# Kernel tuning notes

Hardware: AMD Instinct MI355X
Metric: run time of the kernel (lower is better)

## Reference

```python
import jax, jax.numpy as jnp
import numpy as np

NUM_HEADS = 4
NUM_GROUPS = 8
EPS = 1e-5


def group_norm(x, w, b):
    # x: [N, C, H, W], normalize over (C//G, H, W) per group
    N, C, H, W = x.shape
    xg = x.reshape(N, NUM_GROUPS, C // NUM_GROUPS, H, W)
    mu = jnp.mean(xg, axis=(2, 3, 4), keepdims=True)
    var = jnp.var(xg, axis=(2, 3, 4), keepdims=True)
    xn = ((xg - mu) * jax.lax.rsqrt(var + EPS)).reshape(N, C, H, W)
    return xn * w[None, :, None, None] + b[None, :, None, None]


def conv1x1(x, w, b):
    # x: [N, C, H, W], w: [Cout, Cin], b: [Cout]
    return jnp.einsum('nchw,dc->ndhw', x, w) + b[None, :, None, None]


def setup_inputs() -> dict:
    key = jax.random.key(0)
    ks = jax.random.split(key, 12)
    N, C, H, W = 2, 256, 64, 64
    s = 1.0 / np.sqrt(C)
    inp = {
        'x': jax.random.normal(ks[0], (N, C, H, W), jnp.float32),
        'mask': jax.random.randint(ks[1], (N, 1, H, W), 0, 2, jnp.int32),
        'norm_w': jnp.ones((C,), jnp.float32),
        'norm_b': jnp.zeros((C,), jnp.float32),
        'q_w': jax.random.normal(ks[2], (C, C), jnp.float32) * s,
        'q_b': jnp.zeros((C,), jnp.float32),
        'k_w': jax.random.normal(ks[3], (C, C), jnp.float32) * s,
        'k_b': jnp.zeros((C,), jnp.float32),
        'v_w': jax.random.normal(ks[4], (C, C), jnp.float32) * s,
        'v_b': jnp.zeros((C,), jnp.float32),
        'p_w': jax.random.normal(ks[5], (C, C), jnp.float32) * s,
        'p_b': jnp.zeros((C,), jnp.float32),
    }
    return inp


def reference(x, mask, norm_w, norm_b, q_w, q_b, k_w, k_b, v_w, v_b, p_w, p_b):
    N, C, H, W = x.shape
    hd = C // NUM_HEADS  # head dim
    L = H * W
    xn = group_norm(x, norm_w, norm_b)
    q = conv1x1(xn, q_w, q_b).reshape(N, NUM_HEADS, hd, L)
    k = conv1x1(xn, k_w, k_b).reshape(N, NUM_HEADS, hd, L)
    v = conv1x1(xn, v_w, v_b).reshape(N, NUM_HEADS, hd, L)
    scores = jnp.einsum('nhcl,nhck->nhlk', q, k) * (hd ** -0.5)
    probs = jax.nn.softmax(scores, axis=-1)
    out = jnp.einsum('nhlk,nhck->nhcl', probs, v).reshape(N, C, H, W)
    out = conv1x1(out, p_w, p_b)
    return (x + out, mask)
```

## Files before the change

### kernel.cpp

```cpp
#include <hip/hip_runtime.h>
#include <hip/hip_bf16.h>

#define NBATCH 2
#define CCH    256
#define LLEN   4096
#define NGROUP 8
#define CPG    32
#define NHEAD  4
#define HD     64
#define GEPS   1e-5f
#define QSCALE 0.18033688011112042f


typedef short bf16x8 __attribute__((ext_vector_type(8)));
typedef float f32x4  __attribute__((ext_vector_type(4)));

__device__ __forceinline__ unsigned short f2b(float f) {
  unsigned u = __float_as_uint(f);
  u += 0x7FFFu + ((u >> 16) & 1u);
  return (unsigned short)(u >> 16);
}
__device__ __forceinline__ unsigned pack2bf(float a, float b) {
  __hip_bfloat162 h = __float22bfloat162_rn(make_float2(a, b));
  union { __hip_bfloat162 h; unsigned u; } c;
  c.h = h;
  return c.u;
}
__device__ __forceinline__ float exp2_(float x) {
#if __has_builtin(__builtin_amdgcn_exp2f)
  return __builtin_amdgcn_exp2f(x);
#else
  return exp2f(x);
#endif
}

__global__ __launch_bounds__(256) void setup_kernel(
    const float* __restrict__ qw, const float* __restrict__ kw,
    const float* __restrict__ vw, const float* __restrict__ pw,
    const float* __restrict__ qb, const float* __restrict__ kb,
    const float* __restrict__ vb, const float* __restrict__ pb,
    const float* __restrict__ x, const int* __restrict__ mask,
    unsigned short* __restrict__ w16, float* __restrict__ bias_ws,
    float* __restrict__ part, float* __restrict__ out2) {
  __shared__ float rs[4], rss[4];
  const int b = blockIdx.x;
  const int t = threadIdx.x;
  if (b < 256) {
    const int idx = b * 256 + t;
    const int m = idx >> 14;
    const int rem = idx & 16383;
    const int cout = rem >> 6;
    const int ch4 = (rem & 63) << 2;
    const float* src[4] = {qw, kw, vw, pw};
    const float sc = (m == 0) ? QSCALE : 1.0f;
    const float4 v = ((const float4*)src[m])[(size_t)cout * 64 + (ch4 >> 2)];
    unsigned short* dst = w16 +
        ((size_t)(m * 16 + (cout >> 4)) * 8 + (ch4 >> 5)) * 512 +
        ((cout & 15) + 16 * ((ch4 >> 3) & 3)) * 8 + (ch4 & 7);
    dst[0] = f2b(v.x * sc); dst[1] = f2b(v.y * sc);
    dst[2] = f2b(v.z * sc); dst[3] = f2b(v.w * sc);
    if (b == 0) {
      bias_ws[t]       = qb[t] * QSCALE;
      bias_ws[256 + t] = kb[t];
      bias_ws[512 + t] = vb[t];
      bias_ws[768 + t] = pb[t];
    }
  } else if (b < 384) {
    const int sb = b - 256;
    const int gidx = sb >> 3, sub = sb & 7;
    const float4* xp = (const float4*)(x + (size_t)gidx * (CPG * LLEN)) + (size_t)sub * 4096;
    float s = 0.f, ss = 0.f;
    for (int i = t; i < 4096; i += 256) {
      const float4 v = xp[i];
      s += v.x + v.y + v.z + v.w;
      ss = fmaf(v.x, v.x, ss);
      ss = fmaf(v.y, v.y, ss);
      ss = fmaf(v.z, v.z, ss);
      ss = fmaf(v.w, v.w, ss);
    }
#pragma unroll
    for (int off = 32; off; off >>= 1) {
      s  += __shfl_down(s, off);
      ss += __shfl_down(ss, off);
    }
    if ((t & 63) == 0) { rs[t >> 6] = s; rss[t >> 6] = ss; }
    __syncthreads();
    if (t == 0) {
      part[sb * 2 + 0] = rs[0] + rs[1] + rs[2] + rs[3];
      part[sb * 2 + 1] = rss[0] + rss[1] + rss[2] + rss[3];
    }
  } else {
    const int i = (b - 384) * 256 + t;
    out2[i] = (float)mask[i];
  }
}

__global__ __launch_bounds__(256) void gn_apply_kernel(const float* __restrict__ x,
                                                       const float* __restrict__ w,
                                                       const float* __restrict__ b,
                                                       const float* __restrict__ part,
                                                       unsigned short* __restrict__ xn16) {
  const int l0 = blockIdx.x * 32, c0 = blockIdx.y * 32, n = blockIdx.z;
  const int g16 = n * 8 + (c0 >> 5);
  float s = 0.f, ss = 0.f;
#pragma unroll
  for (int i = 0; i < 8; i++) {
    s  += part[(g16 * 8 + i) * 2 + 0];
    ss += part[(g16 * 8 + i) * 2 + 1];
  }
  const float inv_cnt = 1.0f / (float)(CPG * LLEN);
  const float mu = s * inv_cnt;
  const float rsg = rsqrtf(ss * inv_cnt - mu * mu + GEPS);
  __shared__ float tile[32][33];
  const int tx = threadIdx.x & 31, ty = threadIdx.x >> 5;
#pragma unroll
  for (int i = 0; i < 4; i++) {
    const int c = c0 + ty + 8 * i;
    const float wc = w[c], bc = b[c];
    const float v = x[((size_t)n * CCH + c) * LLEN + l0 + tx];
    tile[ty + 8 * i][tx] = (v - mu) * rsg * wc + bc;
  }
  __syncthreads();
  const int c = c0 + tx;
#pragma unroll
  for (int i = 0; i < 4; i++) {
    const int l = l0 + ty + 8 * i;
    const size_t pos = (((size_t)n * 256 + (l >> 4)) * 8 + (c >> 5)) * 512 +
                       ((l & 15) + 16 * ((c >> 3) & 3)) * 8 + (c & 7);
    xn16[pos] = f2b(tile[tx][ty + 8 * i]);
  }
}

__global__ __launch_bounds__(256, 4) void qkv_mfma_kernel(
    const unsigned short* __restrict__ xn16,
    const unsigned short* __restrict__ w16,
    const float* __restrict__ bias_ws,
    unsigned short* __restrict__ q16,
    unsigned short* __restrict__ k16,
    unsigned short* __restrict__ v16) {
  const int t = threadIdx.x;
  const int lane = t & 63, wv = t >> 6;
  const int col = lane & 15, quad = lane >> 4;
  const int m0 = blockIdx.x * 64;
  const int by = blockIdx.y;
  const int co0 = by * 64;
  const int wsel = blockIdx.z;
  const int n = m0 >> 12;
  const int m16b = (m0 & 4095) >> 4;

  const unsigned short* xnb = xn16 + (size_t)n * (256 * 8 * 512);
  const unsigned short* wb  = w16 + ((size_t)(wsel * 16 + by * 4 + wv) * 8) * 512 + lane * 8;

  f32x4 acc[4];
#pragma unroll
  for (int i = 0; i < 4; i++) acc[i] = {0.f, 0.f, 0.f, 0.f};

#pragma unroll
  for (int kc = 0; kc < 8; kc++) {
    const bf16x8 wf = *(const bf16x8*)(wb + (size_t)kc * 512);
#pragma unroll
    for (int mt = 0; mt < 4; mt++) {
      const bf16x8 xf = *(const bf16x8*)(xnb + ((size_t)(m16b + mt) * 8 + kc) * 512 + lane * 8);
      acc[mt] = (wsel < 2)
          ? __builtin_amdgcn_mfma_f32_16x16x32_bf16(xf, wf, acc[mt], 0, 0, 0)
          : __builtin_amdgcn_mfma_f32_16x16x32_bf16(wf, xf, acc[mt], 0, 0, 0);
    }
  }

  if (wsel < 2) {
    unsigned short* dst = (wsel == 0) ? q16 : k16;
    const float bias = bias_ws[wsel * CCH + co0 + wv * 16 + col];
    const int lquad = (wv * 2 + (col >> 3)) & 3;
    const int j = col & 7;
#pragma unroll
    for (int mt = 0; mt < 4; mt++) {
      const size_t base = ((size_t)(n * 256 + m16b + mt) * 8 + by * 2 + (wv >> 1)) * 512 + j;
#pragma unroll
      for (int r = 0; r < 4; r++)
        dst[base + ((quad * 4 + r) + 16 * lquad) * 8] = f2b(acc[mt][r] + bias);
    }
  } else {
    const int l0 = m0 & 4095;
    const int j = col & 7;
#pragma unroll
    for (int ct = 0; ct < 4; ct++) {
      const size_t base = ((size_t)(n * 128 + (l0 >> 5) + (ct >> 1)) * 16 + by * 4 + wv) * 512 +
                          16 * (((ct & 1) << 1) + (col >> 3)) * 8 + j;
#pragma unroll
      for (int r = 0; r < 4; r++) {
        const int cout = co0 + wv * 16 + quad * 4 + r;
        v16[base + (quad * 4 + r) * 8] = f2b(acc[ct][r] + bias_ws[2 * CCH + cout]);
      }
    }
  }
}

__global__ __launch_bounds__(256, 2) void attn_mfma_kernel(
    const unsigned short* __restrict__ q16,
    const unsigned short* __restrict__ k16,
    const unsigned short* __restrict__ v16,
    unsigned short* __restrict__ o16) {
  __shared__ __align__(16) unsigned char shraw[20480];
  unsigned short (*pT)[64][40] = (unsigned short (*)[64][40])shraw;
  f32x4 (*red)[4][64] = (f32x4 (*)[4][64])shraw;
  f32x4 (*lred)[64] = (f32x4 (*)[64])(shraw + 16384);
  const int t = threadIdx.x;
  const int lane = t & 63, wv = t >> 6;
  const int col = lane & 15, quad = lane >> 4;
  const int q0 = blockIdx.x * 64;
  const int n = blockIdx.y >> 2, h = blockIdx.y & 3;
  const int hc = h * HD;

  const unsigned short* qb = q16 + (size_t)n * (256 * 8 * 512);
  const unsigned short* kb = k16 + (size_t)n * (256 * 8 * 512);
  const unsigned short* vb = v16 + (size_t)n * (128 * 16 * 512);

  bf16x8 bq[4][2];
#pragma unroll
  for (int qt = 0; qt < 4; qt++)
#pragma unroll
    for (int ks = 0; ks < 2; ks++)
      bq[qt][ks] = *(const bf16x8*)(qb + ((size_t)(blockIdx.x * 4 + qt) * 8 + h * 2 + ks) * 512 + lane * 8);

  bf16x8 bones;
#pragma unroll
  for (int i = 0; i < 8; i++) bones[i] = (short)0x3F80;

  f32x4 o[4][4], lacc[4];
#pragma unroll
  for (int qt = 0; qt < 4; qt++) {
    lacc[qt] = {0.f, 0.f, 0.f, 0.f};
#pragma unroll
    for (int ct = 0; ct < 4; ct++) o[qt][ct] = {0.f, 0.f, 0.f, 0.f};
  }

  auto ldK = [&](int kc0, int kt, int ks) {
    return *(const bf16x8*)(kb + ((size_t)((kc0 >> 4) + kt) * 8 + h * 2 + ks) * 512 + lane * 8);
  };
  auto ldV = [&](int kc0, int ct) {
    return *(const bf16x8*)(vb + ((size_t)(kc0 >> 5) * 16 + h * 4 + ct) * 512 + lane * 8);
  };

  int kc0 = wv * 1024;
  bf16x8 ka[2][2], bv[4];
#pragma unroll
  for (int kt = 0; kt < 2; kt++)
#pragma unroll
    for (int ks = 0; ks < 2; ks++) ka[kt][ks] = ldK(kc0, kt, ks);
#pragma unroll
  for (int ct = 0; ct < 4; ct++) bv[ct] = ldV(kc0, ct);

  for (int chunk = 0; chunk < 32; chunk++) {
    const int kn = (chunk < 31) ? kc0 + 32 : kc0;
    bf16x8 nka[2][2], nbv[4];
#pragma unroll
    for (int kt = 0; kt < 2; kt++)
#pragma unroll
      for (int ks = 0; ks < 2; ks++) nka[kt][ks] = ldK(kn, kt, ks);
#pragma unroll
    for (int ct = 0; ct < 4; ct++) nbv[ct] = ldV(kn, ct);

#pragma unroll
    for (int kt = 0; kt < 2; kt++)
#pragma unroll
      for (int qt = 0; qt < 4; qt++) {
        f32x4 s = {0.f, 0.f, 0.f, 0.f};
        s = __builtin_amdgcn_mfma_f32_16x16x32_bf16(ka[kt][0], bq[qt][0], s, 0, 0, 0);
        s = __builtin_amdgcn_mfma_f32_16x16x32_bf16(ka[kt][1], bq[qt][1], s, 0, 0, 0);
        uint2 w;
        w.x = pack2bf(exp2_(s[0]), exp2_(s[1]));
        w.y = pack2bf(exp2_(s[2]), exp2_(s[3]));
        *(uint2*)&pT[wv][qt * 16 + col][kt * 16 + quad * 4] = w;
      }
#pragma unroll
    for (int qt = 0; qt < 4; qt++) {
      const bf16x8 pa = *(const bf16x8*)&pT[wv][qt * 16 + col][quad * 8];
      lacc[qt] = __builtin_amdgcn_mfma_f32_16x16x32_bf16(pa, bones, lacc[qt], 0, 0, 0);
#pragma unroll
      for (int ct = 0; ct < 4; ct++)
        o[qt][ct] = __builtin_amdgcn_mfma_f32_16x16x32_bf16(pa, bv[ct], o[qt][ct], 0, 0, 0);
    }
#pragma unroll
    for (int kt = 0; kt < 2; kt++)
#pragma unroll
      for (int ks = 0; ks < 2; ks++) ka[kt][ks] = nka[kt][ks];
#pragma unroll
    for (int ct = 0; ct < 4; ct++) bv[ct] = nbv[ct];
    kc0 = kn;
  }

  const int cch = hc + wv * 16 + col;
  const int lquad16 = 16 * ((cch >> 3) & 3);
  const size_t ctile = cch >> 5;
#pragma unroll
  for (int qt = 0; qt < 4; qt++) {
    __syncthreads();
#pragma unroll
    for (int ct = 0; ct < 4; ct++) red[wv][ct][lane] = o[qt][ct];
    lred[wv][lane] = lacc[qt];
    __syncthreads();
    f32x4 os = red[0][wv][lane];
    os += red[1][wv][lane];
    os += red[2][wv][lane];
    os += red[3][wv][lane];
    f32x4 ls = lred[0][lane];
    ls += lred[1][lane];
    ls += lred[2][lane];
    ls += lred[3][lane];
    const size_t base = (((size_t)n * 256 + blockIdx.x * 4 + qt) * 8 + ctile) * 512 + (cch & 7);
#pragma unroll
    for (int r = 0; r < 4; r++)
      o16[base + ((quad * 4 + r) + lquad16) * 8] = f2b(os[r] / ls[r]);
  }
}

__global__ __launch_bounds__(256, 4) void proj_mfma_kernel(
    const unsigned short* __restrict__ o16,
    const unsigned short* __restrict__ w16,
    const float* __restrict__ pbias,
    const float* __restrict__ x,
    float* __restrict__ out) {
  const int t = threadIdx.x;
  const int lane = t & 63, wv = t >> 6;
  const int col = lane & 15, quad = lane >> 4;
  const int m0 = blockIdx.x * 64;
  const int by = blockIdx.y;
  const int co0 = by * 64;
  const int n = m0 >> 12, l0 = m0 & 4095;

  const unsigned short* ob = o16 + (size_t)n * (256 * 8 * 512);
  const unsigned short* wb = w16 + ((size_t)(48 + by * 4 + wv) * 8) * 512 + lane * 8;

  f32x4 acc[4];
#pragma unroll
  for (int i = 0; i < 4; i++) acc[i] = {0.f, 0.f, 0.f, 0.f};

#pragma unroll
  for (int kc = 0; kc < 8; kc++) {
    const bf16x8 aw = *(const bf16x8*)(wb + (size_t)kc * 512);
#pragma unroll
    for (int lt = 0; lt < 4; lt++) {
      const bf16x8 bo = *(const bf16x8*)(ob + ((size_t)((l0 >> 4) + lt) * 8 + kc) * 512 + lane * 8);
      acc[lt] = __builtin_amdgcn_mfma_f32_16x16x32_bf16(aw, bo, acc[lt], 0, 0, 0);
    }
  }
#pragma unroll
  for (int lt = 0; lt < 4; lt++)
#pragma unroll
    for (int r = 0; r < 4; r++) {
      const int cout = co0 + wv * 16 + quad * 4 + r;
      const size_t idx = ((size_t)(n * CCH + cout)) * LLEN + l0 + lt * 16 + col;
      out[idx] = acc[lt][r] + pbias[cout] + x[idx];
    }
}

extern "C" void kernel_launch(void* const* d_in, const int* in_sizes, int n_in,
                              void* d_out, int out_size, void* d_ws, size_t ws_size,
                              hipStream_t stream) {
  (void)in_sizes; (void)n_in; (void)out_size; (void)ws_size;
  const float* x      = (const float*)d_in[0];
  const int*   mask   = (const int*)d_in[1];
  const float* norm_w = (const float*)d_in[2];
  const float* norm_b = (const float*)d_in[3];
  const float* q_w    = (const float*)d_in[4];
  const float* q_b    = (const float*)d_in[5];
  const float* k_w    = (const float*)d_in[6];
  const float* k_b    = (const float*)d_in[7];
  const float* v_w    = (const float*)d_in[8];
  const float* v_b    = (const float*)d_in[9];
  const float* p_w    = (const float*)d_in[10];
  const float* p_b    = (const float*)d_in[11];

  const size_t TSZ = (size_t)NBATCH * LLEN * CCH;
  unsigned short* xn16 = (unsigned short*)d_ws;
  unsigned short* q16  = xn16 + TSZ;
  unsigned short* k16  = q16 + TSZ;
  unsigned short* v16  = k16 + TSZ;
  unsigned short* o16  = v16 + TSZ;
  unsigned short* w16  = o16 + TSZ;
  float* bias_ws = (float*)(w16 + 4 * 65536);
  float* part    = bias_ws + 1024;

  float* out  = (float*)d_out;
  float* out2 = out + TSZ;

  setup_kernel<<<416, 256, 0, stream>>>(q_w, k_w, v_w, p_w, q_b, k_b, v_b, p_b,
                                        x, mask, w16, bias_ws, part, out2);
  gn_apply_kernel<<<dim3(LLEN / 32, CCH / 32, NBATCH), 256, 0, stream>>>(
      x, norm_w, norm_b, part, xn16);
  qkv_mfma_kernel<<<dim3((NBATCH * LLEN) / 64, CCH / 64, 3), 256, 0, stream>>>(
      xn16, w16, bias_ws, q16, k16, v16);
  attn_mfma_kernel<<<dim3(LLEN / 64, NBATCH * NHEAD), 256, 0, stream>>>(
      q16, k16, v16, o16);
  proj_mfma_kernel<<<dim3((NBATCH * LLEN) / 64, CCH / 64), 256, 0, stream>>>(
      o16, w16, bias_ws + 768, x, out);
}
```

Before: 154.4 us.

## Halve attention and projection tiles, vectorize groupnorm apply, double-buffer K loads

Attention blocks now cover 32 queries instead of 64, doubling the grid to 1024 blocks. Occupancy is raised to 4 blocks per CU, block IDs are remapped so consecutive blocks share the same head, and the K/V prefetch becomes an explicit ping-pong double buffer. Projection tiles are halved to 32 rows, groupnorm stats are split across more blocks, and gn_apply uses float4 loads with packed bf16x8 stores. The goal is better CU fill on a 256-CU part and cheaper memory traffic, at the cost of less K/V reuse per block and more redundant K/V reads.

```diff
diff --git a/kernel.cpp b/kernel.cpp
--- a/kernel.cpp
+++ b/kernel.cpp
@@ -65,12 +65,12 @@
       bias_ws[512 + t] = vb[t];
       bias_ws[768 + t] = pb[t];
     }
-  } else if (b < 384) {
+  } else if (b < 512) {
     const int sb = b - 256;
-    const int gidx = sb >> 3, sub = sb & 7;
-    const float4* xp = (const float4*)(x + (size_t)gidx * (CPG * LLEN)) + (size_t)sub * 4096;
+    const int gidx = sb >> 4, sub = sb & 15;
+    const float4* xp = (const float4*)(x + (size_t)gidx * (CPG * LLEN)) + (size_t)sub * 2048;
     float s = 0.f, ss = 0.f;
-    for (int i = t; i < 4096; i += 256) {
+    for (int i = t; i < 2048; i += 256) {
       const float4 v = xp[i];
       s += v.x + v.y + v.z + v.w;
       ss = fmaf(v.x, v.x, ss);
@@ -90,7 +90,7 @@
       part[sb * 2 + 1] = rss[0] + rss[1] + rss[2] + rss[3];
     }
   } else {
-    const int i = (b - 384) * 256 + t;
+    const int i = (b - 512) * 256 + t;
     out2[i] = (float)mask[i];
   }
 }
@@ -100,35 +100,42 @@
                                                        const float* __restrict__ b,
                                                        const float* __restrict__ part,
                                                        unsigned short* __restrict__ xn16) {
-  const int l0 = blockIdx.x * 32, c0 = blockIdx.y * 32, n = blockIdx.z;
-  const int g16 = n * 8 + (c0 >> 5);
+  const int l0 = blockIdx.x * 64, c0 = blockIdx.y * 32, n = blockIdx.z;
+  const int g16 = n * 8 + blockIdx.y;
   float s = 0.f, ss = 0.f;
 #pragma unroll
-  for (int i = 0; i < 8; i++) {
-    s  += part[(g16 * 8 + i) * 2 + 0];
-    ss += part[(g16 * 8 + i) * 2 + 1];
+  for (int i = 0; i < 16; i++) {
+    s  += part[(g16 * 16 + i) * 2 + 0];
+    ss += part[(g16 * 16 + i) * 2 + 1];
   }
   const float inv_cnt = 1.0f / (float)(CPG * LLEN);
   const float mu = s * inv_cnt;
   const float rsg = rsqrtf(ss * inv_cnt - mu * mu + GEPS);
-  __shared__ float tile[32][33];
-  const int tx = threadIdx.x & 31, ty = threadIdx.x >> 5;
-#pragma unroll
-  for (int i = 0; i < 4; i++) {
-    const int c = c0 + ty + 8 * i;
-    const float wc = w[c], bc = b[c];
-    const float v = x[((size_t)n * CCH + c) * LLEN + l0 + tx];
-    tile[ty + 8 * i][tx] = (v - mu) * rsg * wc + bc;
+  __shared__ float tile[32][68];
+  const int t = threadIdx.x;
+  const int cl = t >> 3, l8 = t & 7;
+  const float aa = rsg * w[c0 + cl];
+  const float dd = b[c0 + cl] - mu * aa;
+  const float* xrow = x + ((size_t)n * CCH + c0 + cl) * LLEN + l0;
+#pragma unroll
+  for (int i = 0; i < 2; i++) {
+    const int ll = (l8 + 8 * i) * 4;
+    float4 v = *(const float4*)(xrow + ll);
+    v.x = fmaf(v.x, aa, dd);
+    v.y = fmaf(v.y, aa, dd);
+    v.z = fmaf(v.z, aa, dd);
+    v.w = fmaf(v.w, aa, dd);
+    *(float4*)&tile[cl][ll] = v;
   }
   __syncthreads();
-  const int c = c0 + tx;
-#pragma unroll
-  for (int i = 0; i < 4; i++) {
-    const int l = l0 + ty + 8 * i;
-    const size_t pos = (((size_t)n * 256 + (l >> 4)) * 8 + (c >> 5)) * 512 +
-                       ((l & 15) + 16 * ((c >> 3) & 3)) * 8 + (c & 7);
-    xn16[pos] = f2b(tile[tx][ty + 8 * i]);
-  }
+  const int l = t & 63, cg = t >> 6;
+  const int labs = l0 + l;
+  bf16x8 ov;
+#pragma unroll
+  for (int j = 0; j < 8; j++) ov[j] = (short)f2b(tile[cg * 8 + j][l]);
+  const size_t pos = (((size_t)n * 256 + (labs >> 4)) * 8 + (c0 >> 5)) * 512 +
+                     ((labs & 15) + 16 * cg) * 8;
+  *(bf16x8*)(xn16 + pos) = ov;
 }
 
 __global__ __launch_bounds__(256, 4) void qkv_mfma_kernel(
@@ -195,40 +202,42 @@
   }
 }
 
-__global__ __launch_bounds__(256, 2) void attn_mfma_kernel(
+__global__ __launch_bounds__(256, 4) void attn_mfma_kernel(
     const unsigned short* __restrict__ q16,
     const unsigned short* __restrict__ k16,
     const unsigned short* __restrict__ v16,
     unsigned short* __restrict__ o16) {
   __shared__ __align__(16) unsigned char shraw[20480];
-  unsigned short (*pT)[64][40] = (unsigned short (*)[64][40])shraw;
+  unsigned short (*pT)[32][40] = (unsigned short (*)[32][40])shraw;
   f32x4 (*red)[4][64] = (f32x4 (*)[4][64])shraw;
   f32x4 (*lred)[64] = (f32x4 (*)[64])(shraw + 16384);
   const int t = threadIdx.x;
   const int lane = t & 63, wv = t >> 6;
   const int col = lane & 15, quad = lane >> 4;
-  const int q0 = blockIdx.x * 64;
-  const int n = blockIdx.y >> 2, h = blockIdx.y & 3;
+  const int fid = blockIdx.y * gridDim.x + blockIdx.x;
+  const int nh = fid & 7, qx = fid >> 3;
+  const int n = nh >> 2, h = nh & 3;
   const int hc = h * HD;
+  const int qt0 = qx * 2;
 
   const unsigned short* qb = q16 + (size_t)n * (256 * 8 * 512);
   const unsigned short* kb = k16 + (size_t)n * (256 * 8 * 512);
   const unsigned short* vb = v16 + (size_t)n * (128 * 16 * 512);
 
-  bf16x8 bq[4][2];
-#pragma unroll
-  for (int qt = 0; qt < 4; qt++)
+  bf16x8 bq[2][2];
+#pragma unroll
+  for (int qt = 0; qt < 2; qt++)
 #pragma unroll
     for (int ks = 0; ks < 2; ks++)
-      bq[qt][ks] = *(const bf16x8*)(qb + ((size_t)(blockIdx.x * 4 + qt) * 8 + h * 2 + ks) * 512 + lane * 8);
+      bq[qt][ks] = *(const bf16x8*)(qb + ((size_t)(qt0 + qt) * 8 + h * 2 + ks) * 512 + lane * 8);
 
   bf16x8 bones;
 #pragma unroll
   for (int i = 0; i < 8; i++) bones[i] = (short)0x3F80;
 
-  f32x4 o[4][4], lacc[4];
-#pragma unroll
-  for (int qt = 0; qt < 4; qt++) {
+  f32x4 o[2][4], lacc[2];
+#pragma unroll
+  for (int qt = 0; qt < 2; qt++) {
     lacc[qt] = {0.f, 0.f, 0.f, 0.f};
 #pragma unroll
     for (int ct = 0; ct < 4; ct++) o[qt][ct] = {0.f, 0.f, 0.f, 0.f};
@@ -241,59 +250,56 @@
     return *(const bf16x8*)(vb + ((size_t)(kc0 >> 5) * 16 + h * 4 + ct) * 512 + lane * 8);
   };
 
-  int kc0 = wv * 1024;
-  bf16x8 ka[2][2], bv[4];
-#pragma unroll
-  for (int kt = 0; kt < 2; kt++)
-#pragma unroll
-    for (int ks = 0; ks < 2; ks++) ka[kt][ks] = ldK(kc0, kt, ks);
-#pragma unroll
-  for (int ct = 0; ct < 4; ct++) bv[ct] = ldV(kc0, ct);
-
-  for (int chunk = 0; chunk < 32; chunk++) {
-    const int kn = (chunk < 31) ? kc0 + 32 : kc0;
-    bf16x8 nka[2][2], nbv[4];
+  bf16x8 kA[2][2], kB[2][2], bv[4];
+  auto loadK = [&](bf16x8 (&kr)[2][2], int kc0) {
 #pragma unroll
     for (int kt = 0; kt < 2; kt++)
 #pragma unroll
-      for (int ks = 0; ks < 2; ks++) nka[kt][ks] = ldK(kn, kt, ks);
-#pragma unroll
-    for (int ct = 0; ct < 4; ct++) nbv[ct] = ldV(kn, ct);
-
+      for (int ks = 0; ks < 2; ks++) kr[kt][ks] = ldK(kc0, kt, ks);
+  };
+  auto loadV = [&](int kc0) {
+#pragma unroll
+    for (int ct = 0; ct < 4; ct++) bv[ct] = ldV(kc0, ct);
+  };
+  auto chunk = [&](bf16x8 (&kr)[2][2]) {
 #pragma unroll
     for (int kt = 0; kt < 2; kt++)
 #pragma unroll
-      for (int qt = 0; qt < 4; qt++) {
+      for (int qt = 0; qt < 2; qt++) {
         f32x4 s = {0.f, 0.f, 0.f, 0.f};
-        s = __builtin_amdgcn_mfma_f32_16x16x32_bf16(ka[kt][0], bq[qt][0], s, 0, 0, 0);
-        s = __builtin_amdgcn_mfma_f32_16x16x32_bf16(ka[kt][1], bq[qt][1], s, 0, 0, 0);
-        uint2 w;
-        w.x = pack2bf(exp2_(s[0]), exp2_(s[1]));
-        w.y = pack2bf(exp2_(s[2]), exp2_(s[3]));
-        *(uint2*)&pT[wv][qt * 16 + col][kt * 16 + quad * 4] = w;
+        s = __builtin_amdgcn_mfma_f32_16x16x32_bf16(kr[kt][0], bq[qt][0], s, 0, 0, 0);
+        s = __builtin_amdgcn_mfma_f32_16x16x32_bf16(kr[kt][1], bq[qt][1], s, 0, 0, 0);
+        uint2 pw;
+        pw.x = pack2bf(exp2_(s[0]), exp2_(s[1]));
+        pw.y = pack2bf(exp2_(s[2]), exp2_(s[3]));
+        *(uint2*)&pT[wv][qt * 16 + col][kt * 16 + quad * 4] = pw;
       }
 #pragma unroll
-    for (int qt = 0; qt < 4; qt++) {
+    for (int qt = 0; qt < 2; qt++) {
       const bf16x8 pa = *(const bf16x8*)&pT[wv][qt * 16 + col][quad * 8];
       lacc[qt] = __builtin_amdgcn_mfma_f32_16x16x32_bf16(pa, bones, lacc[qt], 0, 0, 0);
 #pragma unroll
       for (int ct = 0; ct < 4; ct++)
         o[qt][ct] = __builtin_amdgcn_mfma_f32_16x16x32_bf16(pa, bv[ct], o[qt][ct], 0, 0, 0);
     }
-#pragma unroll
-    for (int kt = 0; kt < 2; kt++)
-#pragma unroll
-      for (int ks = 0; ks < 2; ks++) ka[kt][ks] = nka[kt][ks];
-#pragma unroll
-    for (int ct = 0; ct < 4; ct++) bv[ct] = nbv[ct];
-    kc0 = kn;
+  };
+
+  const int kb0 = wv * 1024;
+  loadK(kA, kb0);
+  for (int it = 0; it < 32; it += 2) {
+    loadV(kb0 + it * 32);
+    loadK(kB, kb0 + (it + 1) * 32);
+    chunk(kA);
+    loadV(kb0 + (it + 1) * 32);
+    loadK(kA, kb0 + ((it + 2 < 32) ? (it + 2) * 32 : (it + 1) * 32));
+    chunk(kB);
   }
 
   const int cch = hc + wv * 16 + col;
   const int lquad16 = 16 * ((cch >> 3) & 3);
   const size_t ctile = cch >> 5;
 #pragma unroll
-  for (int qt = 0; qt < 4; qt++) {
+  for (int qt = 0; qt < 2; qt++) {
     __syncthreads();
 #pragma unroll
     for (int ct = 0; ct < 4; ct++) red[wv][ct][lane] = o[qt][ct];
@@ -307,7 +313,7 @@
     ls += lred[1][lane];
     ls += lred[2][lane];
     ls += lred[3][lane];
-    const size_t base = (((size_t)n * 256 + blockIdx.x * 4 + qt) * 8 + ctile) * 512 + (cch & 7);
+    const size_t base = (((size_t)n * 256 + qt0 + qt) * 8 + ctile) * 512 + (cch & 7);
 #pragma unroll
     for (int r = 0; r < 4; r++)
       o16[base + ((quad * 4 + r) + lquad16) * 8] = f2b(os[r] / ls[r]);
@@ -323,7 +329,7 @@
   const int t = threadIdx.x;
   const int lane = t & 63, wv = t >> 6;
   const int col = lane & 15, quad = lane >> 4;
-  const int m0 = blockIdx.x * 64;
+  const int m0 = blockIdx.x * 32;
   const int by = blockIdx.y;
   const int co0 = by * 64;
   const int n = m0 >> 12, l0 = m0 & 4095;
@@ -331,21 +337,21 @@
   const unsigned short* ob = o16 + (size_t)n * (256 * 8 * 512);
   const unsigned short* wb = w16 + ((size_t)(48 + by * 4 + wv) * 8) * 512 + lane * 8;
 
-  f32x4 acc[4];
-#pragma unroll
-  for (int i = 0; i < 4; i++) acc[i] = {0.f, 0.f, 0.f, 0.f};
+  f32x4 acc[2];
+#pragma unroll
+  for (int i = 0; i < 2; i++) acc[i] = {0.f, 0.f, 0.f, 0.f};
 
 #pragma unroll
   for (int kc = 0; kc < 8; kc++) {
     const bf16x8 aw = *(const bf16x8*)(wb + (size_t)kc * 512);
 #pragma unroll
-    for (int lt = 0; lt < 4; lt++) {
+    for (int lt = 0; lt < 2; lt++) {
       const bf16x8 bo = *(const bf16x8*)(ob + ((size_t)((l0 >> 4) + lt) * 8 + kc) * 512 + lane * 8);
       acc[lt] = __builtin_amdgcn_mfma_f32_16x16x32_bf16(aw, bo, acc[lt], 0, 0, 0);
     }
   }
 #pragma unroll
-  for (int lt = 0; lt < 4; lt++)
+  for (int lt = 0; lt < 2; lt++)
 #pragma unroll
     for (int r = 0; r < 4; r++) {
       const int cout = co0 + wv * 16 + quad * 4 + r;
@@ -384,14 +390,14 @@
   float* out  = (float*)d_out;
   float* out2 = out + TSZ;
 
-  setup_kernel<<<416, 256, 0, stream>>>(q_w, k_w, v_w, p_w, q_b, k_b, v_b, p_b,
+  setup_kernel<<<544, 256, 0, stream>>>(q_w, k_w, v_w, p_w, q_b, k_b, v_b, p_b,
                                         x, mask, w16, bias_ws, part, out2);
-  gn_apply_kernel<<<dim3(LLEN / 32, CCH / 32, NBATCH), 256, 0, stream>>>(
+  gn_apply_kernel<<<dim3(LLEN / 64, CCH / 32, NBATCH), 256, 0, stream>>>(
       x, norm_w, norm_b, part, xn16);
   qkv_mfma_kernel<<<dim3((NBATCH * LLEN) / 64, CCH / 64, 3), 256, 0, stream>>>(
       xn16, w16, bias_ws, q16, k16, v16);
-  attn_mfma_kernel<<<dim3(LLEN / 64, NBATCH * NHEAD), 256, 0, stream>>>(
+  attn_mfma_kernel<<<dim3(LLEN / 32, NBATCH * NHEAD), 256, 0, stream>>>(
       q16, k16, v16, o16);
-  proj_mfma_kernel<<<dim3((NBATCH * LLEN) / 64, CCH / 64), 256, 0, stream>>>(
+  proj_mfma_kernel<<<dim3((NBATCH * LLEN) / 32, CCH / 64), 256, 0, stream>>>(
       o16, w16, bias_ws + 768, x, out);
 }
```

Result: no change. 156.0 us (+1.0%).
